# Kernel optimization log

Hardware: AMD Instinct MI355X
Metric: run time of the kernel (lower is better)

## Reference

```python
import jax, jax.numpy as jnp
import numpy as np

B, N, DIM, HEADS = 8, 4096, 512, 8
BASE = 10000.0


def rope_cos_sin(n, dim, base=BASE):
    k_max = dim // 2
    theta = 1.0 / base ** (jnp.arange(k_max, dtype=jnp.float32) / k_max)
    angles = jnp.arange(n, dtype=jnp.float32)[:, None] * theta  # (n, k_max)
    return jnp.cos(angles), jnp.sin(angles)


def apply_rope(x, cos, sin):
    # x: (b, n, dim); complex pairs are interleaved (even=real, odd=imag)
    xr = x[..., 0::2]
    xi = x[..., 1::2]
    out_r = cos * xr - sin * xi
    out_i = sin * xr + cos * xi
    return jnp.stack([out_r, out_i], axis=-1).reshape(x.shape)


def setup_inputs() -> dict:
    key = jax.random.key(0)
    ks = jax.random.split(key, 8)
    s = 0.02
    return {
        'x': jax.random.normal(ks[0], (B, N, DIM), jnp.float32),
        'y': jax.random.normal(ks[1], (B, N, DIM), jnp.float32),
        'Wq': jax.random.normal(ks[2], (DIM, DIM), jnp.float32) * s,
        'bq': jax.random.normal(ks[3], (DIM,), jnp.float32) * s,
        'Wk': jax.random.normal(ks[4], (DIM, DIM), jnp.float32) * s,
        'bk': jax.random.normal(ks[5], (DIM,), jnp.float32) * s,
        'lepe_w': jax.random.normal(ks[6], (DIM, 1, 3), jnp.float32) * s,
        'lepe_b': jax.random.normal(ks[7], (DIM,), jnp.float32) * s,
    }


def reference(x, y, Wq, bq, Wk, bk, lepe_w, lepe_b):
    b, n, c = x.shape
    h = HEADS
    d = c // h
    q = jax.nn.elu(x @ Wq.T + bq) + 1.0
    k = jax.nn.elu(y @ Wk.T + bk) + 1.0
    cos, sin = rope_cos_sin(n, c)
    q_rope = apply_rope(q, cos, sin).reshape(b, n, h, d).transpose(0, 2, 1, 3)
    k_rope = apply_rope(k, cos, sin).reshape(b, n, h, d).transpose(0, 2, 1, 3)
    qh = q.reshape(b, n, h, d).transpose(0, 2, 1, 3)
    kh = k.reshape(b, n, h, d).transpose(0, 2, 1, 3)
    v = y.reshape(b, n, h, d).transpose(0, 2, 1, 3)
    kmean = kh.mean(axis=2, keepdims=True)  # (b,h,1,d)
    z = 1.0 / (jnp.einsum('bhnd,bhmd->bhnm', qh, kmean) + 1e-6)  # (b,h,n,1)
    scale = n ** (-0.5)
    kv = jnp.einsum('bhnd,bhne->bhde', k_rope * scale, v * scale)  # (b,h,d,d)
    out = jnp.einsum('bhnd,bhde->bhne', q_rope, kv) * z  # (b,h,n,d)
    out = out.transpose(0, 2, 1, 3).reshape(b, n, c)
    # LePE: depthwise conv1d over value stream
    vc = v.transpose(0, 2, 1, 3).reshape(b, n, c).transpose(0, 2, 1)  # (b,c,n)
    lepe = jax.lax.conv_general_dilated(
        vc, lepe_w, window_strides=(1,), padding=[(1, 1)],
        dimension_numbers=('NCH', 'OIH', 'NCH'), feature_group_count=c)
    lepe = lepe + lepe_b[None, :, None]
    return out + lepe.transpose(0, 2, 1)
```

## Files before the change

kernel.cpp:

```cpp
#include <hip/hip_runtime.h>

#define B_ 8
#define N_ 4096
#define C_ 512
#define H_ 8

typedef _Float16 h8  __attribute__((ext_vector_type(8)));
typedef _Float16 h4v __attribute__((ext_vector_type(4)));
typedef float    f4  __attribute__((ext_vector_type(4)));

static const size_t OFF_CT   = 0;
static const size_t OFF_XH   = (size_t)8*1024*1024;
static const size_t OFF_YH   = (size_t)40*1024*1024;
static const size_t OFF_WQH  = (size_t)72*1024*1024;
static const size_t OFF_WKH  = (size_t)72*1024*1024 + 512*1024;
static const size_t OFF_KSUM = (size_t)73*1024*1024;
static const size_t OFF_KVG  = (size_t)73*1024*1024 + 64*1024;
static const size_t OFF_KVT  = (size_t)74*1024*1024 + 64*1024;

__device__ __forceinline__ unsigned int pack2h(float a, float b){
    union { _Float16 h[2]; unsigned int u; } x;
    x.h[0] = (_Float16)a; x.h[1] = (_Float16)b; return x.u;
}
__device__ __forceinline__ void unpack2h(unsigned int u, float& a, float& b){
    union { unsigned int u; _Float16 h[2]; } x; x.u = u;
    a = (float)x.h[0]; b = (float)x.h[1];
}

__global__ __launch_bounds__(256) void k_tables(unsigned int* __restrict__ ct){
    int jj = blockIdx.x, t = threadIdx.x;
    double th = exp((double)jj * -0.035977892078031970);
    float thf = (float)th;
#pragma unroll
    for (int i=0;i<16;++i){
        int n = i*256 + t;
        float s, c; sincosf((float)n * thf, &s, &c);
        ct[(size_t)jj*4096 + n] = pack2h(c, s);
    }
}

__global__ __launch_bounds__(256) void k_prep(
    const float* __restrict__ y, const float* __restrict__ x,
    const float* __restrict__ Wq, const float* __restrict__ Wk,
    _Float16* __restrict__ yh, _Float16* __restrict__ xh,
    _Float16* __restrict__ Wqh, _Float16* __restrict__ Wkh)
{
    int bid = blockIdx.x;
    const float* src; _Float16* dst; size_t base;
    if (bid < 8192)       { src = y;  dst = yh;  base = (size_t)bid*2048; }
    else if (bid < 16384) { src = x;  dst = xh;  base = (size_t)(bid-8192)*2048; }
    else if (bid < 16512) { src = Wq; dst = Wqh; base = (size_t)(bid-16384)*2048; }
    else                  { src = Wk; dst = Wkh; base = (size_t)(bid-16512)*2048; }
    size_t o = base + (size_t)threadIdx.x*8;
    float4 a = *(const float4*)&src[o];
    float4 b = *(const float4*)&src[o+4];
    uint4 r; r.x = pack2h(a.x,a.y); r.y = pack2h(a.z,a.w); r.z = pack2h(b.x,b.y); r.w = pack2h(b.z,b.w);
    *(uint4*)&dst[o] = r;
}

__device__ __forceinline__ void stage_a64(const _Float16* __restrict__ g, _Float16* lds, int t){
    int r = t >> 2;
    int j = (t & 3) ^ ((r ^ (r >> 2)) & 3);
    __builtin_amdgcn_global_load_lds(
        (const __attribute__((address_space(1))) void*)(g + (size_t)r*C_ + j*8),
        (__attribute__((address_space(3))) void*)(lds + (size_t)(t & 192)*8),
        16, 0, 0);
}
__device__ __forceinline__ void stage_b128(const _Float16* __restrict__ g, _Float16* lds, int t){
#pragma unroll
    for (int i=0;i<2;++i){
        int u = i*256 + t;
        int r = u >> 2;
        int j = (u & 3) ^ ((r ^ (r >> 2)) & 3);
        __builtin_amdgcn_global_load_lds(
            (const __attribute__((address_space(1))) void*)(g + (size_t)r*C_ + j*8),
            (__attribute__((address_space(3))) void*)(lds + (size_t)(i*256 + (t & 192))*8),
            16, 0, 0);
    }
}

template<int IS_Q>
__global__ __launch_bounds__(256, 4) void k_gemm(
    const _Float16* __restrict__ A, const _Float16* __restrict__ Wh, const float* __restrict__ bias,
    const unsigned int* __restrict__ ct,
    float* __restrict__ ksum, const float* __restrict__ ksumIn,
    float* __restrict__ kvg, const _Float16* __restrict__ kvTg,
    const _Float16* __restrict__ yh, const float* __restrict__ lw, const float* __restrict__ lb,
    float* __restrict__ outp)
{
    __shared__ __align__(16) char smem[36864];
    _Float16* qrs = (_Float16*)smem;
    unsigned int* krsU = (unsigned int*)smem;
    unsigned int* vsU  = (unsigned int*)(smem + 16384);

    const int t = threadIdx.x;
    const int lane = t & 63;
    const int w = t >> 6;
    const int wm = w >> 1, wn = w & 1;
    const int d_lin = blockIdx.x + (blockIdx.y << 2);
    const int xcd = d_lin & 7;
    const int sq  = d_lin >> 3;
    const int col0 = (sq & 3) * 128;
    const int row0 = (xcd * 64 + (sq >> 2)) * 64;
    const int lrow = lane & 15, lg = lane >> 4;
    const int b = row0 >> 12;

    f4 acc[2][4] = {};
    const _Float16* Ab = A  + (size_t)row0*C_;
    const _Float16* Bb = Wh + (size_t)col0*C_;
    stage_a64 (Ab,      (_Float16*)(smem),               t);
    stage_b128(Bb,      (_Float16*)(smem + 12288),       t);
    stage_a64 (Ab + 32, (_Float16*)(smem + 4096),        t);
    stage_b128(Bb + 32, (_Float16*)(smem + 12288 + 8192),t);

    const int sw = (lrow ^ (lrow >> 2)) & 3;
    const int cK = (lg ^ sw) * 8;

#pragma unroll
    for (int kk=0; kk<16; ++kk){
        if (kk < 15) asm volatile("s_waitcnt vmcnt(3)" ::: "memory");
        else         asm volatile("s_waitcnt vmcnt(0)" ::: "memory");
        __builtin_amdgcn_s_barrier();
        if (kk < 14){
            const int ss = (kk+2)%3;
            stage_a64 (Ab + (kk+2)*32, (_Float16*)(smem + ss*4096),         t);
            stage_b128(Bb + (kk+2)*32, (_Float16*)(smem + 12288 + ss*8192), t);
        }
        const int sc = kk%3;
        const _Float16* As = (const _Float16*)(smem + sc*4096);
        const _Float16* Bs = (const _Float16*)(smem + 12288 + sc*8192);
        h8 af[2], bf[4];
#pragma unroll
        for (int mi=0; mi<2; ++mi) af[mi] = *(const h8*)&As[(wm*32 + mi*16 + lrow)*32 + cK];
#pragma unroll
        for (int ni=0; ni<4; ++ni) bf[ni] = *(const h8*)&Bs[(wn*64 + ni*16 + lrow)*32 + cK];
#pragma unroll
        for (int mi=0; mi<2; ++mi)
#pragma unroll
            for (int ni=0; ni<4; ++ni)
                acc[mi][ni] = __builtin_amdgcn_mfma_f32_16x16x32_f16(af[mi], bf[ni], acc[mi][ni], 0,0,0);
    }
    __syncthreads();

    const int hcol0 = col0 + wn*64;
    float bcol[4], km[4];
#pragma unroll
    for (int ni=0; ni<4; ++ni){
        int c = hcol0 + ni*16 + lrow;
        bcol[ni] = bias[c];
        km[ni] = IS_Q ? ksumIn[b*C_ + c] * (1.0f/4096.0f) : 0.0f;
    }
    float colsum[4] = {0.f,0.f,0.f,0.f};
    float zr[2][4];
    _Float16* qw = qrs + w*2304;

#pragma unroll
    for (int mi=0; mi<2; ++mi){
        float qv[4][4];
#pragma unroll
        for (int ni=0; ni<4; ++ni)
#pragma unroll
            for (int r=0; r<4; ++r){
                float v = acc[mi][ni][r] + bcol[ni];
                qv[ni][r] = v > 0.f ? v + 1.f : __expf(v);
            }
        if constexpr (IS_Q){
#pragma unroll
            for (int r=0; r<4; ++r){
                float p = qv[0][r]*km[0] + qv[1][r]*km[1] + qv[2][r]*km[2] + qv[3][r]*km[3];
                p += __shfl_xor(p, 1); p += __shfl_xor(p, 2);
                p += __shfl_xor(p, 4); p += __shfl_xor(p, 8);
                zr[mi][r] = 1.0f / (p + 1e-6f);
            }
        } else {
#pragma unroll
            for (int ni=0; ni<4; ++ni)
                colsum[ni] += qv[ni][0]+qv[ni][1]+qv[ni][2]+qv[ni][3];
        }
        const int n0 = (row0 & (N_-1)) + wm*32 + mi*16 + lg*4;
#pragma unroll
        for (int ni=0; ni<4; ++ni){
            int c = hcol0 + ni*16 + lrow;
            int jj = c >> 1;
            uint4 tu = *(const uint4*)&ct[(size_t)jj*4096 + n0];
            float cs4[4], sn4[4];
            unpack2h(tu.x, cs4[0], sn4[0]);
            unpack2h(tu.y, cs4[1], sn4[1]);
            unpack2h(tu.z, cs4[2], sn4[2]);
            unpack2h(tu.w, cs4[3], sn4[3]);
            float rv[4];
#pragma unroll
            for (int r=0; r<4; ++r){
                float val = qv[ni][r];
                float par = __shfl_xor(val, 1);
                rv[r] = (lane & 1) ? fmaf(sn4[r], par, cs4[r]*val) : fmaf(cs4[r], val, -sn4[r]*par);
            }
            if constexpr (IS_Q){
#pragma unroll
                for (int r=0; r<4; ++r){
                    float prv = __shfl_xor(rv[r], 1);
                    if (!(lane & 1))
                        *(unsigned int*)&qw[(mi*16 + lg*4 + r)*72 + (ni*16 + lrow)] = pack2h(rv[r], prv);
                }
            } else {
                int d = ni*16 + lrow;
                int n2 = wm*16 + mi*8 + lg*2;
                unsigned int* p = &krsU[wn*2048 + d*32 + (n2 ^ ((d & 7) << 2))];
                uint2 pr; pr.x = pack2h(rv[0], rv[1]); pr.y = pack2h(rv[2], rv[3]);
                *(uint2*)p = pr;
            }
        }
    }

    if constexpr (!IS_Q){
#pragma unroll
        for (int ni=0; ni<4; ++ni){
            float s = colsum[ni];
            s += __shfl_xor(s, 16); s += __shfl_xor(s, 32);
            if (lane < 16) atomicAdd(&ksum[b*C_ + hcol0 + ni*16 + lane], s);
        }
        {
            const int grp = lane >> 4, li = lane & 15;
#pragma unroll
            for (int it=0; it<8; ++it){
                int g = it*4 + w;
                int hl = g >> 4, q = g & 15;
                int row = q*4 + grp;
                uint2 mine = *(const uint2*)&yh[(size_t)(row0 + row)*C_ + col0 + hl*64 + li*4];
                uint2 oth; oth.x = __shfl_xor(mine.x, 16); oth.y = __shfl_xor(mine.y, 16);
                if (!(grp & 1)){
                    int n2 = row >> 1;
#pragma unroll
                    for (int e=0; e<4; ++e){
                        int ea = li*4 + e;
                        unsigned int mf = ((e<2 ? mine.x : mine.y) >> ((e&1)*16)) & 0xffffu;
                        unsigned int of = ((e<2 ? oth.x  : oth.y ) >> ((e&1)*16)) & 0xffffu;
                        vsU[hl*2048 + ea*32 + (n2 ^ ((ea & 7) << 2))] = mf | (of << 16);
                    }
                }
            }
        }
        __syncthreads();
        f4 acc2[2][4] = {};
        const unsigned int* krsW = krsU + wn*2048;
        const unsigned int* vsW  = vsU  + wn*2048;
#pragma unroll
        for (int ks=0; ks<2; ++ks){
            h8 a2[2], b2[4];
#pragma unroll
            for (int mi2=0; mi2<2; ++mi2){
                int d = wm*32 + mi2*16 + lrow;
                int c4 = (ks*16 + lg*4) ^ ((d & 7) << 2);
                a2[mi2] = *(const h8*)&krsW[d*32 + c4];
            }
#pragma unroll
            for (int ni2=0; ni2<4; ++ni2){
                int e = ni2*16 + lrow;
                int c4 = (ks*16 + lg*4) ^ ((e & 7) << 2);
                b2[ni2] = *(const h8*)&vsW[e*32 + c4];
            }
#pragma unroll
            for (int mi2=0; mi2<2; ++mi2)
#pragma unroll
                for (int ni2=0; ni2<4; ++ni2)
                    acc2[mi2][ni2] = __builtin_amdgcn_mfma_f32_16x16x32_f16(a2[mi2], b2[ni2], acc2[mi2][ni2], 0,0,0);
        }
        const int bh = b*H_ + (col0 >> 6) + wn;
#pragma unroll
        for (int mi2=0; mi2<2; ++mi2)
#pragma unroll
            for (int ni2=0; ni2<4; ++ni2)
#pragma unroll
                for (int rr=0; rr<4; ++rr){
                    int d = wm*32 + mi2*16 + lg*4 + rr;
                    int e = ni2*16 + lrow;
                    atomicAdd(&kvg[(size_t)bh*4096 + d*64 + e], acc2[mi2][ni2][rr] * (1.0f/4096.0f));
                }
    } else {
        const int bhh = b*H_ + (col0 >> 6) + wn;
        h8 kv0[4], kv1[4];
#pragma unroll
        for (int ni2=0; ni2<4; ++ni2){
            int e = ni2*16 + lrow;
            kv0[ni2] = *(const h8*)&kvTg[(size_t)bhh*4096 + e*64 + lg*8];
            kv1[ni2] = *(const h8*)&kvTg[(size_t)bhh*4096 + e*64 + 32 + lg*8];
        }
        __syncthreads();
        f4 acc2[2][4] = {};
#pragma unroll
        for (int mi2=0; mi2<2; ++mi2){
            h8 a0 = *(const h8*)&qw[(mi2*16 + lrow)*72 + 0*32 + lg*8];
            h8 a1 = *(const h8*)&qw[(mi2*16 + lrow)*72 + 1*32 + lg*8];
#pragma unroll
            for (int ni2=0; ni2<4; ++ni2){
                acc2[mi2][ni2] = __builtin_amdgcn_mfma_f32_16x16x32_f16(a0, kv0[ni2], acc2[mi2][ni2], 0,0,0);
                acc2[mi2][ni2] = __builtin_amdgcn_mfma_f32_16x16x32_f16(a1, kv1[ni2], acc2[mi2][ni2], 0,0,0);
            }
        }
#pragma unroll
        for (int mi2=0; mi2<2; ++mi2){
#pragma unroll
            for (int r=0; r<4; ++r){
                float z = zr[mi2][r];
#pragma unroll
                for (int ni2=0; ni2<4; ++ni2){
                    float val = acc2[mi2][ni2][r] * z;
                    float pv = __shfl_xor(val, 1);
                    if (!(lane & 1))
                        *(unsigned int*)&qw[(mi2*16 + lg*4 + r)*72 + (ni2*16 + lrow)] = pack2h(val, pv);
                }
            }
        }
        __syncthreads();
        const int cg = t & 31;
        const int c4p = cg * 4;
        const int hl = c4p >> 6;
        const int e0 = c4p & 63;
        float w0[4], w1[4], w2[4], wb[4];
#pragma unroll
        for (int j=0;j<4;++j){
            int cc = col0 + c4p + j;
            w0[j]=lw[cc*3+0]; w1[j]=lw[cc*3+1]; w2[j]=lw[cc*3+2]; wb[j]=lb[cc];
        }
#pragma unroll
        for (int i=0;i<8;++i){
            int rl = (t >> 5) + i*8;
            int grow = row0 + rl;
            int nloc = grow & (N_-1);
            int wreg = ((rl >> 5) << 1) + hl;
            h4v a = *(const h4v*)&qrs[wreg*2304 + (rl & 31)*72 + e0];
            const _Float16* yp = yh + (size_t)grow*C_ + col0 + c4p;
            h4v y1 = *(const h4v*)yp;
            float s0 = fmaf((float)y1[0], w1[0], wb[0]);
            float s1 = fmaf((float)y1[1], w1[1], wb[1]);
            float s2 = fmaf((float)y1[2], w1[2], wb[2]);
            float s3 = fmaf((float)y1[3], w1[3], wb[3]);
            if (nloc > 0){
                h4v y0 = *(const h4v*)(yp - C_);
                s0 = fmaf((float)y0[0], w0[0], s0); s1 = fmaf((float)y0[1], w0[1], s1);
                s2 = fmaf((float)y0[2], w0[2], s2); s3 = fmaf((float)y0[3], w0[3], s3);
            }
            if (nloc < N_-1){
                h4v y2 = *(const h4v*)(yp + C_);
                s0 = fmaf((float)y2[0], w2[0], s0); s1 = fmaf((float)y2[1], w2[1], s1);
                s2 = fmaf((float)y2[2], w2[2], s2); s3 = fmaf((float)y2[3], w2[3], s3);
            }
            float4 o;
            o.x = (float)a[0] + s0; o.y = (float)a[1] + s1;
            o.z = (float)a[2] + s2; o.w = (float)a[3] + s3;
            *(float4*)&outp[(size_t)grow*C_ + col0 + c4p] = o;
        }
    }
}

__global__ __launch_bounds__(256) void k_kvmerge(const float* __restrict__ kvg, _Float16* __restrict__ kvTg){
    int bh = blockIdx.x, t = threadIdx.x;
    const float* src = kvg + (size_t)bh*4096;
    _Float16* dst = kvTg + (size_t)bh*4096;
#pragma unroll
    for (int i=0;i<4;++i){
        int q = i*256 + t;
        int e2 = q & 31, d2 = q >> 5;
        float2 a0 = *(const float2*)&src[(2*d2)*64 + 2*e2];
        float2 a1 = *(const float2*)&src[(2*d2+1)*64 + 2*e2];
        *(unsigned int*)&dst[(2*e2)*64 + 2*d2]   = pack2h(a0.x, a1.x);
        *(unsigned int*)&dst[(2*e2+1)*64 + 2*d2] = pack2h(a0.y, a1.y);
    }
}

extern "C" void kernel_launch(void* const* d_in, const int* in_sizes, int n_in,
                              void* d_out, int out_size, void* d_ws, size_t ws_size,
                              hipStream_t stream)
{
    (void)in_sizes; (void)n_in; (void)out_size; (void)ws_size;
    const float* x  = (const float*)d_in[0];
    const float* y  = (const float*)d_in[1];
    const float* Wq = (const float*)d_in[2];
    const float* bq = (const float*)d_in[3];
    const float* Wk = (const float*)d_in[4];
    const float* bk = (const float*)d_in[5];
    const float* lw = (const float*)d_in[6];
    const float* lb = (const float*)d_in[7];

    char* ws = (char*)d_ws;
    unsigned int* ct = (unsigned int*)(ws + OFF_CT);
    _Float16* xh   = (_Float16*)(ws + OFF_XH);
    _Float16* yh   = (_Float16*)(ws + OFF_YH);
    _Float16* Wqh  = (_Float16*)(ws + OFF_WQH);
    _Float16* Wkh  = (_Float16*)(ws + OFF_WKH);
    float*    ksum = (float*)(ws + OFF_KSUM);
    float*    kvg  = (float*)(ws + OFF_KVG);
    _Float16* kvTg = (_Float16*)(ws + OFF_KVT);
    float*    out  = (float*)d_out;

    hipMemsetAsync(ws + OFF_KSUM, 0, 64*1024 + 1024*1024, stream);
    k_tables<<<dim3(256), dim3(256), 0, stream>>>(ct);
    k_prep<<<dim3(16640), dim3(256), 0, stream>>>(y, x, Wq, Wk, yh, xh, Wqh, Wkh);
    k_gemm<0><<<dim3(4, 512), dim3(256), 0, stream>>>(yh, Wkh, bk, ct,
        ksum, nullptr, kvg, nullptr, yh, nullptr, nullptr, nullptr);
    k_kvmerge<<<dim3(64), dim3(256), 0, stream>>>(kvg, kvTg);
    k_gemm<1><<<dim3(4, 512), dim3(256), 0, stream>>>(xh, Wqh, bq, ct,
        nullptr, ksum, nullptr, kvTg, yh, lw, lb, out);
}
```

Before: 188.5 us.

## Fold table generation into prep and overlap x conversion with K GEMM

Merges the cos/sin table kernel into the prep kernel as extra blocks, removing one launch. The fp32-to-fp16 conversion of x moves out of prep and into 256 extra blocks appended to the K-projection GEMM grid, so it runs alongside the GEMM tiles instead of ahead of them. This cuts serialized memory-bound work and launch overhead. The extra conversion blocks may compete with GEMM tiles for bandwidth and CU slots, and any workgroup-ID-based tile mapping must still hold for the enlarged grid.

```diff
diff --git a/kernel.cpp b/kernel.cpp
--- a/kernel.cpp
+++ b/kernel.cpp
@@ -27,30 +27,30 @@
     a = (float)x.h[0]; b = (float)x.h[1];
 }
 
-__global__ __launch_bounds__(256) void k_tables(unsigned int* __restrict__ ct){
-    int jj = blockIdx.x, t = threadIdx.x;
-    double th = exp((double)jj * -0.035977892078031970);
-    float thf = (float)th;
-#pragma unroll
-    for (int i=0;i<16;++i){
-        int n = i*256 + t;
-        float s, c; sincosf((float)n * thf, &s, &c);
-        ct[(size_t)jj*4096 + n] = pack2h(c, s);
-    }
-}
-
 __global__ __launch_bounds__(256) void k_prep(
-    const float* __restrict__ y, const float* __restrict__ x,
+    const float* __restrict__ y,
     const float* __restrict__ Wq, const float* __restrict__ Wk,
-    _Float16* __restrict__ yh, _Float16* __restrict__ xh,
-    _Float16* __restrict__ Wqh, _Float16* __restrict__ Wkh)
+    _Float16* __restrict__ yh,
+    _Float16* __restrict__ Wqh, _Float16* __restrict__ Wkh,
+    unsigned int* __restrict__ ct)
 {
     int bid = blockIdx.x;
+    if (bid >= 8448){
+        int jj = bid - 8448, t = threadIdx.x;
+        double th = exp((double)jj * -0.035977892078031970);
+        float thf = (float)th;
+#pragma unroll
+        for (int i=0;i<16;++i){
+            int n = i*256 + t;
+            float s, c; sincosf((float)n * thf, &s, &c);
+            ct[(size_t)jj*4096 + n] = pack2h(c, s);
+        }
+        return;
+    }
     const float* src; _Float16* dst; size_t base;
     if (bid < 8192)       { src = y;  dst = yh;  base = (size_t)bid*2048; }
-    else if (bid < 16384) { src = x;  dst = xh;  base = (size_t)(bid-8192)*2048; }
-    else if (bid < 16512) { src = Wq; dst = Wqh; base = (size_t)(bid-16384)*2048; }
-    else                  { src = Wk; dst = Wkh; base = (size_t)(bid-16512)*2048; }
+    else if (bid < 8320)  { src = Wq; dst = Wqh; base = (size_t)(bid-8192)*2048; }
+    else                  { src = Wk; dst = Wkh; base = (size_t)(bid-8320)*2048; }
     size_t o = base + (size_t)threadIdx.x*8;
     float4 a = *(const float4*)&src[o];
     float4 b = *(const float4*)&src[o+4];
@@ -86,12 +86,29 @@
     float* __restrict__ ksum, const float* __restrict__ ksumIn,
     float* __restrict__ kvg, const _Float16* __restrict__ kvTg,
     const _Float16* __restrict__ yh, const float* __restrict__ lw, const float* __restrict__ lb,
-    float* __restrict__ outp)
+    float* __restrict__ outp,
+    const float* __restrict__ x32, _Float16* __restrict__ xh16)
 {
     __shared__ __align__(16) char smem[36864];
     _Float16* qrs = (_Float16*)smem;
     unsigned int* krsU = (unsigned int*)smem;
     unsigned int* vsU  = (unsigned int*)(smem + 16384);
+
+    if constexpr (!IS_Q){
+        if (blockIdx.y >= 512){
+            int cb = (blockIdx.y - 512)*4 + blockIdx.x;
+#pragma unroll 4
+            for (int it=0; it<32; ++it){
+                size_t o = ((size_t)(cb*32 + it))*2048 + (size_t)threadIdx.x*8;
+                float4 a = *(const float4*)&x32[o];
+                float4 b = *(const float4*)&x32[o+4];
+                uint4 r; r.x = pack2h(a.x,a.y); r.y = pack2h(a.z,a.w);
+                r.z = pack2h(b.x,b.y); r.w = pack2h(b.z,b.w);
+                *(uint4*)&xh16[o] = r;
+            }
+            return;
+        }
+    }
 
     const int t = threadIdx.x;
     const int lane = t & 63;
@@ -394,11 +411,10 @@
     float*    out  = (float*)d_out;
 
     hipMemsetAsync(ws + OFF_KSUM, 0, 64*1024 + 1024*1024, stream);
-    k_tables<<<dim3(256), dim3(256), 0, stream>>>(ct);
-    k_prep<<<dim3(16640), dim3(256), 0, stream>>>(y, x, Wq, Wk, yh, xh, Wqh, Wkh);
-    k_gemm<0><<<dim3(4, 512), dim3(256), 0, stream>>>(yh, Wkh, bk, ct,
-        ksum, nullptr, kvg, nullptr, yh, nullptr, nullptr, nullptr);
+    k_prep<<<dim3(8704), dim3(256), 0, stream>>>(y, Wq, Wk, yh, Wqh, Wkh, ct);
+    k_gemm<0><<<dim3(4, 576), dim3(256), 0, stream>>>(yh, Wkh, bk, ct,
+        ksum, nullptr, kvg, nullptr, yh, nullptr, nullptr, nullptr, x, xh);
     k_kvmerge<<<dim3(64), dim3(256), 0, stream>>>(kvg, kvTg);
     k_gemm<1><<<dim3(4, 512), dim3(256), 0, stream>>>(xh, Wqh, bq, ct,
-        nullptr, ksum, nullptr, kvTg, yh, lw, lb, out);
-}
+        nullptr, ksum, nullptr, kvTg, yh, lw, lb, out, nullptr, nullptr);
+}
```

Measured after the change: 185.2 us. About the same (-1.8%).
